# Kernel tuning notes

Measured on AMD Instinct MI355X. Metric: run time of the kernel, lower is better.

The kernel has to match this reference:

```python
import jax, jax.numpy as jnp
import numpy as np

N_NODES = 100000
N_EDGES = 800000
N_REL = 16
D = 64
EPS = 1e-12
NEG_SLOPE = 0.01  # nn.LeakyReLU default


def _l2norm(x):
    # matches torch F.normalize(p=2, dim=-1)
    n = jnp.sqrt(jnp.sum(x * x, axis=-1, keepdims=True))
    return x / jnp.maximum(n, EPS)


def setup_inputs() -> dict:
    key = jax.random.key(0)
    ks = jax.random.split(key, 12)
    inp = {
        "src": jax.random.randint(ks[0], (N_EDGES,), 0, N_NODES, dtype=jnp.int32),
        "dst": jax.random.randint(ks[1], (N_EDGES,), 0, N_NODES, dtype=jnp.int32),
        "etype": jax.random.randint(ks[2], (N_EDGES,), 0, N_REL, dtype=jnp.int32),
        "ent_embed": jax.random.normal(ks[3], (N_NODES, D), jnp.float32) * 0.1,
        "ent_transfer": jax.random.normal(ks[4], (N_NODES, D), jnp.float32) * 0.1,
        "rel_embed": jax.random.normal(ks[5], (N_REL, D), jnp.float32) * 0.1,
        "rel_transfer": jax.random.normal(ks[6], (N_REL, D), jnp.float32) * 0.1,
        "W1_0": jax.random.normal(ks[7], (64, 32), jnp.float32) * (1.0 / np.sqrt(64)),
        "b1_0": jnp.zeros((32,), jnp.float32),
        "W2_0": jax.random.normal(ks[8], (64, 32), jnp.float32) * (1.0 / np.sqrt(64)),
        "b2_0": jnp.zeros((32,), jnp.float32),
        "W1_1": jax.random.normal(ks[9], (32, 16), jnp.float32) * (1.0 / np.sqrt(32)),
        "b1_1": jnp.zeros((16,), jnp.float32),
        "W2_1": jax.random.normal(ks[10], (32, 16), jnp.float32) * (1.0 / np.sqrt(32)),
        "b2_1": jnp.zeros((16,), jnp.float32),
    }
    return inp


def _compute_att(src, dst, etype, ent_embed, ent_transfer, rel_embed, rel_transfer):
    # per-edge gathers: h = dst node, t = src node (KGAT att_score convention)
    h_e = ent_embed[dst]          # [E, D]
    t_e = ent_embed[src]          # [E, D]
    h_p = ent_transfer[dst]
    t_p = ent_transfer[src]
    r_p = rel_transfer[etype]     # [E, D]
    r_e = rel_embed[etype]        # [E, D]
    # TransD projection + L2 normalize
    Mrt = _l2norm(t_e + jnp.sum(t_e * t_p, -1, keepdims=True) * r_p)
    Mrh = _l2norm(h_e + jnp.sum(h_e * h_p, -1, keepdims=True) * r_p)
    att = jnp.sum(Mrt * jnp.tanh(Mrh + r_e), axis=-1)  # [E]
    # edge softmax grouped by destination node
    m = jax.ops.segment_max(att, dst, num_segments=N_NODES)
    m = jnp.where(jnp.isfinite(m), m, 0.0)
    ex = jnp.exp(att - m[dst])
    s = jax.ops.segment_sum(ex, dst, num_segments=N_NODES)
    return ex / jnp.maximum(s[dst], EPS)  # [E]


def _bi_layer(node, N_h, W1, b1, W2, b2):
    out1 = jax.nn.leaky_relu((node + N_h) @ W1 + b1, NEG_SLOPE)
    out2 = jax.nn.leaky_relu((node * N_h) @ W2 + b2, NEG_SLOPE)
    return out1 + out2


def reference(src, dst, etype, ent_embed, ent_transfer, rel_embed, rel_transfer,
              W1_0, b1_0, W2_0, b2_0, W1_1, b1_1, W2_1, b2_1):
    att = _compute_att(src, dst, etype, ent_embed, ent_transfer, rel_embed, rel_transfer)
    node = ent_embed
    all_embed = [node]
    for (W1, b1, W2, b2) in [(W1_0, b1_0, W2_0, b2_0), (W1_1, b1_1, W2_1, b2_1)]:
        # u_mul_e + sum: N_h[v] = sum_{e: dst(e)=v} att_e * node[src(e)]
        msg = att[:, None] * node[src]                      # [E, d]
        N_h = jax.ops.segment_sum(msg, dst, num_segments=N_NODES)
        node = _bi_layer(node, N_h, W1, b1, W2, b2)         # dropout p=0 (eval)
        all_embed.append(_l2norm(node))
    return jnp.concatenate(all_embed, axis=1)  # [N, 64+32+16]
```

## Files before the change

kernel.cpp:

```cpp
#include <hip/hip_runtime.h>
#include <math.h>

#define EPSF 1e-12f
#define LOG2E 1.44269504f

template <int CTRL>
__device__ __forceinline__ float dppadd(float x) {
    union { float f; int i; } u, r;
    u.f = x;
    r.i = __builtin_amdgcn_update_dpp(0, u.i, CTRL, 0xF, 0xF, false);
    return x + r.f;
}
__device__ __forceinline__ float red16(float v) {
    v = dppadd<0xB1>(v); v = dppadd<0x4E>(v);
    v = dppadd<0x141>(v); v = dppadd<0x140>(v);
    return v;
}
__device__ __forceinline__ float red8(float v) {
    v = dppadd<0xB1>(v); v = dppadd<0x4E>(v); v = dppadd<0x141>(v);
    return v;
}
__device__ __forceinline__ float xor8add(float v) {
    return dppadd<0x128>(v);
}

__device__ __forceinline__ float fast_tanh(float x) {
    float E = __builtin_amdgcn_exp2f(x * (2.0f * LOG2E));
    return 1.0f - 2.0f * __builtin_amdgcn_rcpf(E + 1.0f);
}

__device__ __forceinline__ float inv_norm(float x) {
    return __builtin_amdgcn_rsqf(fmaxf(x, 1e-24f));
}

__device__ __forceinline__ float leaky(float x) {
    return x > 0.0f ? x : 0.01f * x;
}

__global__ __launch_bounds__(256) void prep(
    const float* __restrict__ ent, const float* __restrict__ entT,
    float* __restrict__ dot, const int* __restrict__ dst,
    int* __restrict__ deg, int N16, int E,
    const float* __restrict__ W10, const float* __restrict__ W20,
    const float* __restrict__ W11, const float* __restrict__ W21,
    float4* __restrict__ wt) {
    int gid = blockIdx.x * 256 + threadIdx.x;
    if (gid < N16) {
        int v = gid >> 4, lane = gid & 15;
        const float4 a = *(const float4*)(ent  + (size_t)v * 64 + lane * 4);
        const float4 b = *(const float4*)(entT + (size_t)v * 64 + lane * 4);
        float d = red16(a.x*b.x + a.y*b.y + a.z*b.z + a.w*b.w);
        if (lane == 0) dot[v] = d;
    } else if (gid < N16 + E) {
        int e = gid - N16;
        atomicAdd(&deg[dst[e]], 1);
    } else {
        int w = gid - N16 - E;
        if (w < 512) {
            int dd = w >> 5, j = w & 31, d4 = dd * 4;
            wt[w] = make_float4(W10[(d4+0)*32+j], W10[(d4+1)*32+j],
                                W10[(d4+2)*32+j], W10[(d4+3)*32+j]);
        } else if (w < 1024) {
            int u = w - 512, dd = u >> 5, j = u & 31, d4 = dd * 4;
            wt[w] = make_float4(W20[(d4+0)*32+j], W20[(d4+1)*32+j],
                                W20[(d4+2)*32+j], W20[(d4+3)*32+j]);
        } else if (w < 1152) {
            int u = w - 1024, dd = u >> 4, j = u & 15, d4 = dd * 4;
            wt[w] = make_float4(W11[(d4+0)*16+j], W11[(d4+1)*16+j],
                                W11[(d4+2)*16+j], W11[(d4+3)*16+j]);
        } else if (w < 1280) {
            int u = w - 1152, dd = u >> 4, j = u & 15, d4 = dd * 4;
            wt[w] = make_float4(W21[(d4+0)*16+j], W21[(d4+1)*16+j],
                                W21[(d4+2)*16+j], W21[(d4+3)*16+j]);
        }
    }
}


__global__ __launch_bounds__(256) void scan_reduce(
    const int* __restrict__ deg, int* __restrict__ part, int N) {
    __shared__ int sh[256];
    int t = threadIdx.x, i = blockIdx.x * 256 + t;
    sh[t] = (i < N) ? deg[i] : 0;
    __syncthreads();
    for (int off = 128; off > 0; off >>= 1) {
        if (t < off) sh[t] += sh[t + off];
        __syncthreads();
    }
    if (t == 0) part[blockIdx.x] = sh[0];
}

__global__ __launch_bounds__(1024) void scan_part(int* __restrict__ part, int nb) {
    __shared__ int sh[1024];
    int t = threadIdx.x;
    int x = (t < nb) ? part[t] : 0;
    sh[t] = x;
    __syncthreads();
    for (int off = 1; off < 1024; off <<= 1) {
        int y = (t >= off) ? sh[t - off] : 0;
        __syncthreads();
        sh[t] += y;
        __syncthreads();
    }
    if (t < nb) part[t] = sh[t] - x;
}

__global__ __launch_bounds__(256) void scan_write(
    int* __restrict__ rowptr, const int* __restrict__ part, int N) {
    __shared__ int sh[256];
    int t = threadIdx.x, i = blockIdx.x * 256 + t;
    int x = (i < N) ? rowptr[i] : 0;
    sh[t] = x;
    __syncthreads();
    for (int off = 1; off < 256; off <<= 1) {
        int y = (t >= off) ? sh[t - off] : 0;
        __syncthreads();
        sh[t] += y;
        __syncthreads();
    }
    if (i < N) rowptr[i] = part[blockIdx.x] + sh[t] - x;
}

__global__ __launch_bounds__(256) void scatter_edges(
    const int* __restrict__ src, const int* __restrict__ dst,
    const int* __restrict__ ety, const float* __restrict__ dot,
    int* __restrict__ rowptr, int2* __restrict__ spk2, int E) {
    int e = blockIdx.x * 256 + threadIdx.x;
    if (e < E) {
        int sv = src[e];
        int slot = atomicAdd(&rowptr[dst[e]], 1);
        spk2[slot] = make_int2(sv | (ety[e] << 20), __float_as_int(dot[sv]));
    }
}

__global__ __launch_bounds__(256) void fused_l0(
    const int* __restrict__ rowptr, const int2* __restrict__ spk2,
    const float* __restrict__ ent, const float* __restrict__ dot,
    const float* __restrict__ relE, const float* __restrict__ relT,
    const float4* __restrict__ wt,
    const float* __restrict__ b1, const float* __restrict__ b2,
    float* __restrict__ exatt, float* __restrict__ sinv,
    float* __restrict__ node1raw, float* __restrict__ out, int N) {
    __shared__ float  al[8][64];
    __shared__ float  bl[8][64];
    __shared__ float  rT[16][64];
    __shared__ float  rE[16][64];
    __shared__ float4 WtA[512];
    __shared__ float4 WtB[512];
    int t = threadIdx.x;

    {
        int r = t >> 4, c = (t & 15) * 4;
        *(float4*)&rT[r][c] = *(const float4*)(relT + r * 64 + c);
        *(float4*)&rE[r][c] = *(const float4*)(relE + r * 64 + c);
        WtA[t]       = wt[t];
        WtA[t + 256] = wt[t + 256];
        WtB[t]       = wt[512 + t];
        WtB[t + 256] = wt[768 + t];
    }
    __syncthreads();

    int nv = t >> 5, half = (t >> 4) & 1, lane = t & 15;
    int v = blockIdx.x * 8 + nv;
    if (v >= N) return;

    int s = v ? rowptr[v - 1] : 0;
    int epos = rowptr[v];
    int deg = epos - s;
    int mid = s + ((deg + 1) >> 1);
    int hs   = half ? mid  : s;
    int hend = half ? epos : mid;

    const float4 he = *(const float4*)(ent + (size_t)v * 64 + lane * 4);
    float dh = dot[v];

    float4 macc = {0.f, 0.f, 0.f, 0.f};
    float sumex = 0.0f;

    for (int base = hs; base < hend; base += 16) {
        int rem = hend - base;
        int cnt = rem < 16 ? rem : 16;
        int2 ms = spk2[base + (lane < rem ? lane : rem - 1)];
        float myex = 0.0f;

        int pk0 = __shfl(ms.x, 0, 16);
        int pk1 = __shfl(ms.x, cnt > 1 ? 1 : 0, 16);
        float sd0 = __int_as_float(__shfl(ms.y, 0, 16));
        float sd1 = __int_as_float(__shfl(ms.y, cnt > 1 ? 1 : 0, 16));
        float4 te0 = *(const float4*)(ent + (size_t)(pk0 & 0xFFFFF) * 64 + lane * 4);
        float4 te1 = *(const float4*)(ent + (size_t)(pk1 & 0xFFFFF) * 64 + lane * 4);

        for (int k = 0; k < cnt; k += 2) {
            float4 ta = te0, tb = te1;
            float  sa = sd0, sb = sd1;
            int rva = (pk0 >> 20) & 15;
            int rvb = (pk1 >> 20) & 15;
            bool hasb = (k + 1) < cnt;

            if (k + 2 < cnt) {
                int i2 = k + 2, i3 = (k + 3 < cnt) ? (k + 3) : (k + 2);
                pk0 = __shfl(ms.x, i2, 16);
                pk1 = __shfl(ms.x, i3, 16);
                sd0 = __int_as_float(__shfl(ms.y, i2, 16));
                sd1 = __int_as_float(__shfl(ms.y, i3, 16));
                te0 = *(const float4*)(ent + (size_t)(pk0 & 0xFFFFF) * 64 + lane * 4);
                te1 = *(const float4*)(ent + (size_t)(pk1 & 0xFFFFF) * 64 + lane * 4);
            }

            const float4 rpa = *(const float4*)&rT[rva][lane * 4];
            const float4 rea = *(const float4*)&rE[rva][lane * 4];
            const float4 rpb = *(const float4*)&rT[rvb][lane * 4];
            const float4 reb = *(const float4*)&rE[rvb][lane * 4];

            float4 mta, mha, mtb, mhb;
            mta.x = ta.x + sa * rpa.x; mta.y = ta.y + sa * rpa.y;
            mta.z = ta.z + sa * rpa.z; mta.w = ta.w + sa * rpa.w;
            mha.x = he.x + dh * rpa.x; mha.y = he.y + dh * rpa.y;
            mha.z = he.z + dh * rpa.z; mha.w = he.w + dh * rpa.w;
            mtb.x = tb.x + sb * rpb.x; mtb.y = tb.y + sb * rpb.y;
            mtb.z = tb.z + sb * rpb.z; mtb.w = tb.w + sb * rpb.w;
            mhb.x = he.x + dh * rpb.x; mhb.y = he.y + dh * rpb.y;
            mhb.z = he.z + dh * rpb.z; mhb.w = he.w + dh * rpb.w;

            float ssta = red16(mta.x*mta.x + mta.y*mta.y + mta.z*mta.z + mta.w*mta.w);
            float ssha = red16(mha.x*mha.x + mha.y*mha.y + mha.z*mha.z + mha.w*mha.w);
            float sstb = red16(mtb.x*mtb.x + mtb.y*mtb.y + mtb.z*mtb.z + mtb.w*mtb.w);
            float sshb = red16(mhb.x*mhb.x + mhb.y*mhb.y + mhb.z*mhb.z + mhb.w*mhb.w);
            float ita = inv_norm(ssta), iha = inv_norm(ssha);
            float itb = inv_norm(sstb), ihb = inv_norm(sshb);

            float txa = fast_tanh(mha.x * iha + rea.x);
            float tya = fast_tanh(mha.y * iha + rea.y);
            float tza = fast_tanh(mha.z * iha + rea.z);
            float twa = fast_tanh(mha.w * iha + rea.w);
            float txb = fast_tanh(mhb.x * ihb + reb.x);
            float tyb = fast_tanh(mhb.y * ihb + reb.y);
            float tzb = fast_tanh(mhb.z * ihb + reb.z);
            float twb = fast_tanh(mhb.w * ihb + reb.w);

            float atta = ita * red16(mta.x*txa + mta.y*tya + mta.z*tza + mta.w*twa);
            float attb = itb * red16(mtb.x*txb + mtb.y*tyb + mtb.z*tzb + mtb.w*twb);

            float exa  = __builtin_amdgcn_exp2f(atta * LOG2E);
            float exbR = __builtin_amdgcn_exp2f(attb * LOG2E);
            float exb  = hasb ? exbR : 0.0f;

            myex = (lane == k) ? exa : myex;
            myex = (lane == k + 1) ? exbR : myex;

            sumex += exa + exb;
            macc.x += exa * ta.x + exb * tb.x;
            macc.y += exa * ta.y + exb * tb.y;
            macc.z += exa * ta.z + exb * tb.z;
            macc.w += exa * ta.w + exb * tb.w;
        }
        if (lane < cnt) exatt[base + lane] = myex;
    }

    sumex  += __shfl_xor(sumex,  16, 32);
    macc.x += __shfl_xor(macc.x, 16, 32);
    macc.y += __shfl_xor(macc.y, 16, 32);
    macc.z += __shfl_xor(macc.z, 16, 32);
    macc.w += __shfl_xor(macc.w, 16, 32);

    float inv = 1.0f / fmaxf(sumex, EPSF);
    if ((t & 31) == 0) sinv[v] = inv;
    macc.x *= inv; macc.y *= inv; macc.z *= inv; macc.w *= inv;

    if (!half) {
        *(float4*)(out + (size_t)v * 112 + lane * 4) = he;
        float4 av, bv;
        av.x = he.x + macc.x; av.y = he.y + macc.y;
        av.z = he.z + macc.z; av.w = he.w + macc.w;
        bv.x = he.x * macc.x; bv.y = he.y * macc.y;
        bv.z = he.z * macc.z; bv.w = he.w * macc.w;
        *(float4*)&al[nv][lane * 4] = av;
        *(float4*)&bl[nv][lane * 4] = bv;
    }

    int j = t & 31;
    float acc1 = b1[j], acc2 = b2[j];
    #pragma unroll
    for (int dd = 0; dd < 16; ++dd) {
        float4 a4 = *(const float4*)&al[nv][dd * 4];
        float4 b4 = *(const float4*)&bl[nv][dd * 4];
        float4 wa = WtA[dd * 32 + j];
        float4 wb = WtB[dd * 32 + j];
        acc1 += a4.x*wa.x + a4.y*wa.y + a4.z*wa.z + a4.w*wa.w;
        acc2 += b4.x*wb.x + b4.y*wb.y + b4.z*wb.z + b4.w*wb.w;
    }
    node1raw[(size_t)v * 32 + j] = leaky(acc1) + leaky(acc2);
}

__global__ __launch_bounds__(256) void fused_l1(
    const int* __restrict__ rowptr, const int2* __restrict__ spk2,
    const float* __restrict__ exatt, const float* __restrict__ sinv,
    const float* __restrict__ node1raw, const float4* __restrict__ wt,
    const float* __restrict__ b1, const float* __restrict__ b2,
    float* __restrict__ out, int N) {
    __shared__ float  A[16][32];
    __shared__ float  B[16][32];
    __shared__ float4 WtC[128];
    __shared__ float4 WtD[128];
    int t = threadIdx.x;

    {
        if (t < 128) WtC[t] = wt[1024 + t];
        else WtD[t - 128] = wt[1024 + t];
    }
    __syncthreads();

    int nv = t >> 4, half = (t >> 3) & 1, lane = t & 7;
    int v = blockIdx.x * 16 + nv;
    if (v >= N) return;

    int s = v ? rowptr[v - 1] : 0;
    int epos = rowptr[v];
    int deg = epos - s;
    int mid = s + ((deg + 1) >> 1);
    int hs   = half ? mid  : s;
    int hend = half ? epos : mid;

    float4 n = *(const float4*)(node1raw + (size_t)v * 32 + lane * 4);
    float4 acc = {0.f, 0.f, 0.f, 0.f};

    for (int base = hs; base < hend; base += 8) {
        int rem = hend - base;
        int cnt = rem < 8 ? rem : 8;
        int idx = base + (lane < rem ? lane : rem - 1);
        int   mypk = spk2[idx].x;
        float myex = exatt[idx];

        int pk0 = __shfl(mypk, 0, 8);
        int pk1 = __shfl(mypk, cnt > 1 ? 1 : 0, 8);
        float4 x0 = *(const float4*)(node1raw + (size_t)(pk0 & 0xFFFFF) * 32 + lane * 4);
        float4 x1 = *(const float4*)(node1raw + (size_t)(pk1 & 0xFFFFF) * 32 + lane * 4);

        for (int k = 0; k < cnt; k += 2) {
            float4 xa = x0, xb = x1;
            float aa = __shfl(myex, k, 8);
            float ab = __shfl(myex, (k + 1 < cnt) ? (k + 1) : k, 8);
            if (!((k + 1) < cnt)) ab = 0.0f;

            if (k + 2 < cnt) {
                pk0 = __shfl(mypk, k + 2, 8);
                pk1 = __shfl(mypk, (k + 3 < cnt) ? (k + 3) : (k + 2), 8);
                x0 = *(const float4*)(node1raw + (size_t)(pk0 & 0xFFFFF) * 32 + lane * 4);
                x1 = *(const float4*)(node1raw + (size_t)(pk1 & 0xFFFFF) * 32 + lane * 4);
            }
            acc.x += aa * xa.x + ab * xb.x;
            acc.y += aa * xa.y + ab * xb.y;
            acc.z += aa * xa.z + ab * xb.z;
            acc.w += aa * xa.w + ab * xb.w;
        }
    }
    acc.x = xor8add(acc.x);
    acc.y = xor8add(acc.y);
    acc.z = xor8add(acc.z);
    acc.w = xor8add(acc.w);

    float inv = sinv[v];
    acc.x *= inv; acc.y *= inv; acc.z *= inv; acc.w *= inv;

    float ss = red8(n.x*n.x + n.y*n.y + n.z*n.z + n.w*n.w);
    float inv1 = inv_norm(ss);

    if (!half) {
        float4 nn = {n.x*inv1, n.y*inv1, n.z*inv1, n.w*inv1};
        *(float4*)(out + (size_t)v * 112 + 64 + lane * 4) = nn;
        float4 av = {n.x + acc.x, n.y + acc.y, n.z + acc.z, n.w + acc.w};
        float4 bv = {n.x * acc.x, n.y * acc.y, n.z * acc.z, n.w * acc.w};
        *(float4*)&A[nv][lane * 4] = av;
        *(float4*)&B[nv][lane * 4] = bv;
    }

    int j = t & 15;
    float a1 = b1[j], a2 = b2[j];
    #pragma unroll
    for (int dd = 0; dd < 8; ++dd) {
        float4 a4 = *(const float4*)&A[nv][dd * 4];
        float4 b4 = *(const float4*)&B[nv][dd * 4];
        float4 wc = WtC[dd * 16 + j];
        float4 wd = WtD[dd * 16 + j];
        a1 += a4.x*wc.x + a4.y*wc.y + a4.z*wc.z + a4.w*wc.w;
        a2 += b4.x*wd.x + b4.y*wd.y + b4.z*wd.z + b4.w*wd.w;
    }
    float tot = leaky(a1) + leaky(a2);
    float s2 = red16(tot * tot);
    float inv2 = inv_norm(s2);
    out[(size_t)v * 112 + 96 + j] = tot * inv2;
}

extern "C" void kernel_launch(void* const* d_in, const int* in_sizes, int n_in,
                              void* d_out, int out_size, void* d_ws, size_t ws_size,
                              hipStream_t stream) {
    const int*   src  = (const int*)d_in[0];
    const int*   dst  = (const int*)d_in[1];
    const int*   ety  = (const int*)d_in[2];
    const float* ent  = (const float*)d_in[3];
    const float* entT = (const float*)d_in[4];
    const float* relE = (const float*)d_in[5];
    const float* relT = (const float*)d_in[6];
    const float* W1_0 = (const float*)d_in[7];
    const float* b1_0 = (const float*)d_in[8];
    const float* W2_0 = (const float*)d_in[9];
    const float* b2_0 = (const float*)d_in[10];
    const float* W1_1 = (const float*)d_in[11];
    const float* b1_1 = (const float*)d_in[12];
    const float* W2_1 = (const float*)d_in[13];
    const float* b2_1 = (const float*)d_in[14];
    float* out = (float*)d_out;

    const int E = in_sizes[0];
    const int N = in_sizes[3] / 64;
    const int nb = (N + 255) / 256;

    auto al256 = [](size_t x) { return (x + 255) & ~(size_t)255; };
    char* ws = (char*)d_ws;
    size_t offExatt = 0;
    size_t offS     = al256(offExatt + (size_t)E * 4);
    size_t offDot   = al256(offS + (size_t)N * 4);
    size_t offRow   = al256(offDot + (size_t)N * 4);
    size_t offSpk   = al256(offRow + (size_t)N * 4);
    size_t offPart  = al256(offSpk + (size_t)E * 8);
    size_t offN1    = al256(offPart + (size_t)nb * 4);
    size_t offWt    = al256(offN1 + (size_t)N * 32 * 4);
    float*  exatt    = (float*)(ws + offExatt);
    float*  sinv     = (float*)(ws + offS);
    float*  dot      = (float*)(ws + offDot);
    int*    rowptr   = (int*)(ws + offRow);
    int2*   spk2     = (int2*)(ws + offSpk);
    int*    part     = (int*)(ws + offPart);
    float*  node1raw = (float*)(ws + offN1);
    float4* wt       = (float4*)(ws + offWt);

    hipMemsetAsync(rowptr, 0, (size_t)N * 4, stream);
    int N16 = N * 16;
    int prepWork = N16 + E + 1280;
    prep<<<(prepWork + 255) / 256, 256, 0, stream>>>(
        ent, entT, dot, dst, rowptr, N16, E, W1_0, W2_0, W1_1, W2_1, wt);
    scan_reduce<<<nb, 256, 0, stream>>>(rowptr, part, N);
    scan_part<<<1, 1024, 0, stream>>>(part, nb);
    scan_write<<<nb, 256, 0, stream>>>(rowptr, part, N);
    int blkE = (E + 255) / 256;
    scatter_edges<<<blkE, 256, 0, stream>>>(src, dst, ety, dot, rowptr, spk2, E);

    fused_l0<<<(N + 7) / 8, 256, 0, stream>>>(
        rowptr, spk2, ent, dot, relE, relT,
        wt, b1_0, b2_0, exatt, sinv, node1raw, out, N);

    fused_l1<<<(N + 15) / 16, 256, 0, stream>>>(
        rowptr, spk2, exatt, sinv, node1raw, wt,
        b1_1, b2_1, out, N);
}
```

Measured before the change: 207.8 us.

## Precompute TransD projection norms algebraically per edge instead of reducing in-kernel

Expands the squared norm of e + (e·p)·r as |e|² + 2(e·p)(e·r) + (e·p)²|r|², so the per-edge inverse norms come from per-node dot products against the 16 relation vectors plus per-relation norms. Prep now computes |e|² per node and a node×relation table of e·r, and scatter_edges computes both inverse norms per edge and stores them in a widened 16-byte edge record. This removes four 16-lane DPP reductions per edge pair from fused_l0. In exchange the edge records are twice as large, so fused_l0 and fused_l1 read more bytes, scatter_edges does extra random gathers, and the expanded form can lose precision through cancellation.

```diff
diff --git a/kernel.cpp b/kernel.cpp
--- a/kernel.cpp
+++ b/kernel.cpp
@@ -39,8 +39,10 @@
 
 __global__ __launch_bounds__(256) void prep(
     const float* __restrict__ ent, const float* __restrict__ entT,
-    float* __restrict__ dot, const int* __restrict__ dst,
+    float2* __restrict__ dn, const int* __restrict__ dst,
     int* __restrict__ deg, int N16, int E,
+    const float* __restrict__ relT, float* __restrict__ hrp,
+    float* __restrict__ rp2,
     const float* __restrict__ W10, const float* __restrict__ W20,
     const float* __restrict__ W11, const float* __restrict__ W21,
     float4* __restrict__ wt) {
@@ -49,13 +51,36 @@
         int v = gid >> 4, lane = gid & 15;
         const float4 a = *(const float4*)(ent  + (size_t)v * 64 + lane * 4);
         const float4 b = *(const float4*)(entT + (size_t)v * 64 + lane * 4);
-        float d = red16(a.x*b.x + a.y*b.y + a.z*b.z + a.w*b.w);
-        if (lane == 0) dot[v] = d;
+        float d  = red16(a.x*b.x + a.y*b.y + a.z*b.z + a.w*b.w);
+        float n2 = red16(a.x*a.x + a.y*a.y + a.z*a.z + a.w*a.w);
+        if (lane == 0) dn[v] = make_float2(d, n2);
     } else if (gid < N16 + E) {
         int e = gid - N16;
         atomicAdd(&deg[dst[e]], 1);
+    } else if (gid < N16 + E + N16) {
+        int idx = gid - N16 - E;
+        int n = idx >> 4, r = idx & 15;
+        const float4* e4 = (const float4*)(ent + (size_t)n * 64);
+        const float4* w4 = (const float4*)(relT + r * 64);
+        float acc = 0.0f;
+        #pragma unroll
+        for (int k = 0; k < 16; ++k) {
+            float4 a = e4[k], b = w4[k];
+            acc += a.x*b.x + a.y*b.y + a.z*b.z + a.w*b.w;
+        }
+        hrp[n * 16 + r] = acc;
+    } else if (gid < N16 + E + N16 + 16) {
+        int r = gid - N16 - E - N16;
+        const float4* w4 = (const float4*)(relT + r * 64);
+        float acc = 0.0f;
+        #pragma unroll
+        for (int k = 0; k < 16; ++k) {
+            float4 b = w4[k];
+            acc += b.x*b.x + b.y*b.y + b.z*b.z + b.w*b.w;
+        }
+        rp2[r] = acc;
     } else {
-        int w = gid - N16 - E;
+        int w = gid - N16 - E - N16 - 16;
         if (w < 512) {
             int dd = w >> 5, j = w & 31, d4 = dd * 4;
             wt[w] = make_float4(W10[(d4+0)*32+j], W10[(d4+1)*32+j],
@@ -123,19 +148,29 @@
 
 __global__ __launch_bounds__(256) void scatter_edges(
     const int* __restrict__ src, const int* __restrict__ dst,
-    const int* __restrict__ ety, const float* __restrict__ dot,
-    int* __restrict__ rowptr, int2* __restrict__ spk2, int E) {
+    const int* __restrict__ ety, const float2* __restrict__ dn,
+    const float* __restrict__ hrp, const float* __restrict__ rp2,
+    int* __restrict__ rowptr, int4* __restrict__ spk4, int E) {
     int e = blockIdx.x * 256 + threadIdx.x;
     if (e < E) {
-        int sv = src[e];
-        int slot = atomicAdd(&rowptr[dst[e]], 1);
-        spk2[slot] = make_int2(sv | (ety[e] << 20), __float_as_int(dot[sv]));
+        int sv = src[e], dv = dst[e], rv = ety[e];
+        float2 dns = dn[sv], dnd = dn[dv];
+        float hs = hrp[sv * 16 + rv], hd = hrp[dv * 16 + rv];
+        float r2 = rp2[rv];
+        float sdt = dns.x, dh = dnd.x;
+        float sst = dns.y + 2.0f * sdt * hs + sdt * sdt * r2;
+        float ssh = dnd.y + 2.0f * dh  * hd + dh  * dh  * r2;
+        float it = inv_norm(sst);
+        float ih = inv_norm(ssh);
+        int slot = atomicAdd(&rowptr[dv], 1);
+        spk4[slot] = make_int4(sv | (rv << 20), __float_as_int(sdt),
+                               __float_as_int(it), __float_as_int(ih));
     }
 }
 
 __global__ __launch_bounds__(256) void fused_l0(
-    const int* __restrict__ rowptr, const int2* __restrict__ spk2,
-    const float* __restrict__ ent, const float* __restrict__ dot,
+    const int* __restrict__ rowptr, const int4* __restrict__ spk4,
+    const float* __restrict__ ent, const float2* __restrict__ dn,
     const float* __restrict__ relE, const float* __restrict__ relT,
     const float4* __restrict__ wt,
     const float* __restrict__ b1, const float* __restrict__ b2,
@@ -172,7 +207,7 @@
     int hend = half ? epos : mid;
 
     const float4 he = *(const float4*)(ent + (size_t)v * 64 + lane * 4);
-    float dh = dot[v];
+    float dh = dn[v].x;
 
     float4 macc = {0.f, 0.f, 0.f, 0.f};
     float sumex = 0.0f;
@@ -180,19 +215,25 @@
     for (int base = hs; base < hend; base += 16) {
         int rem = hend - base;
         int cnt = rem < 16 ? rem : 16;
-        int2 ms = spk2[base + (lane < rem ? lane : rem - 1)];
+        int4 ms = spk4[base + (lane < rem ? lane : rem - 1)];
         float myex = 0.0f;
 
-        int pk0 = __shfl(ms.x, 0, 16);
-        int pk1 = __shfl(ms.x, cnt > 1 ? 1 : 0, 16);
+        int e1i = cnt > 1 ? 1 : 0;
+        int   pk0 = __shfl(ms.x, 0, 16);
+        int   pk1 = __shfl(ms.x, e1i, 16);
         float sd0 = __int_as_float(__shfl(ms.y, 0, 16));
-        float sd1 = __int_as_float(__shfl(ms.y, cnt > 1 ? 1 : 0, 16));
+        float sd1 = __int_as_float(__shfl(ms.y, e1i, 16));
+        float it0 = __int_as_float(__shfl(ms.z, 0, 16));
+        float it1 = __int_as_float(__shfl(ms.z, e1i, 16));
+        float ih0 = __int_as_float(__shfl(ms.w, 0, 16));
+        float ih1 = __int_as_float(__shfl(ms.w, e1i, 16));
         float4 te0 = *(const float4*)(ent + (size_t)(pk0 & 0xFFFFF) * 64 + lane * 4);
         float4 te1 = *(const float4*)(ent + (size_t)(pk1 & 0xFFFFF) * 64 + lane * 4);
 
         for (int k = 0; k < cnt; k += 2) {
             float4 ta = te0, tb = te1;
             float  sa = sd0, sb = sd1;
+            float ita = it0, itb = it1, iha = ih0, ihb = ih1;
             int rva = (pk0 >> 20) & 15;
             int rvb = (pk1 >> 20) & 15;
             bool hasb = (k + 1) < cnt;
@@ -203,6 +244,10 @@
                 pk1 = __shfl(ms.x, i3, 16);
                 sd0 = __int_as_float(__shfl(ms.y, i2, 16));
                 sd1 = __int_as_float(__shfl(ms.y, i3, 16));
+                it0 = __int_as_float(__shfl(ms.z, i2, 16));
+                it1 = __int_as_float(__shfl(ms.z, i3, 16));
+                ih0 = __int_as_float(__shfl(ms.w, i2, 16));
+                ih1 = __int_as_float(__shfl(ms.w, i3, 16));
                 te0 = *(const float4*)(ent + (size_t)(pk0 & 0xFFFFF) * 64 + lane * 4);
                 te1 = *(const float4*)(ent + (size_t)(pk1 & 0xFFFFF) * 64 + lane * 4);
             }
@@ -221,13 +266,6 @@
             mtb.z = tb.z + sb * rpb.z; mtb.w = tb.w + sb * rpb.w;
             mhb.x = he.x + dh * rpb.x; mhb.y = he.y + dh * rpb.y;
             mhb.z = he.z + dh * rpb.z; mhb.w = he.w + dh * rpb.w;
-
-            float ssta = red16(mta.x*mta.x + mta.y*mta.y + mta.z*mta.z + mta.w*mta.w);
-            float ssha = red16(mha.x*mha.x + mha.y*mha.y + mha.z*mha.z + mha.w*mha.w);
-            float sstb = red16(mtb.x*mtb.x + mtb.y*mtb.y + mtb.z*mtb.z + mtb.w*mtb.w);
-            float sshb = red16(mhb.x*mhb.x + mhb.y*mhb.y + mhb.z*mhb.z + mhb.w*mhb.w);
-            float ita = inv_norm(ssta), iha = inv_norm(ssha);
-            float itb = inv_norm(sstb), ihb = inv_norm(sshb);
 
             float txa = fast_tanh(mha.x * iha + rea.x);
             float tya = fast_tanh(mha.y * iha + rea.y);
@@ -293,7 +331,7 @@
 }
 
 __global__ __launch_bounds__(256) void fused_l1(
-    const int* __restrict__ rowptr, const int2* __restrict__ spk2,
+    const int* __restrict__ rowptr, const int4* __restrict__ spk4,
     const float* __restrict__ exatt, const float* __restrict__ sinv,
     const float* __restrict__ node1raw, const float4* __restrict__ wt,
     const float* __restrict__ b1, const float* __restrict__ b2,
@@ -328,7 +366,7 @@
         int rem = hend - base;
         int cnt = rem < 8 ? rem : 8;
         int idx = base + (lane < rem ? lane : rem - 1);
-        int   mypk = spk2[idx].x;
+        int   mypk = spk4[idx].x;
         float myex = exatt[idx];
 
         int pk0 = __shfl(mypk, 0, 8);
@@ -418,38 +456,44 @@
     auto al256 = [](size_t x) { return (x + 255) & ~(size_t)255; };
     char* ws = (char*)d_ws;
     size_t offExatt = 0;
-    size_t offS     = al256(offExatt + (size_t)E * 4);
-    size_t offDot   = al256(offS + (size_t)N * 4);
-    size_t offRow   = al256(offDot + (size_t)N * 4);
+    size_t offDn    = al256(offExatt + (size_t)E * 4);
+    size_t offS     = al256(offDn + (size_t)N * 8);
+    size_t offRow   = al256(offS + (size_t)N * 4);
     size_t offSpk   = al256(offRow + (size_t)N * 4);
-    size_t offPart  = al256(offSpk + (size_t)E * 8);
+    size_t offHrp   = al256(offSpk + (size_t)E * 16);
+    size_t offRp2   = al256(offHrp + (size_t)N * 16 * 4);
+    size_t offPart  = al256(offRp2 + 16 * 4);
     size_t offN1    = al256(offPart + (size_t)nb * 4);
     size_t offWt    = al256(offN1 + (size_t)N * 32 * 4);
     float*  exatt    = (float*)(ws + offExatt);
+    float2* dn       = (float2*)(ws + offDn);
     float*  sinv     = (float*)(ws + offS);
-    float*  dot      = (float*)(ws + offDot);
     int*    rowptr   = (int*)(ws + offRow);
-    int2*   spk2     = (int2*)(ws + offSpk);
+    int4*   spk4     = (int4*)(ws + offSpk);
+    float*  hrp      = (float*)(ws + offHrp);
+    float*  rp2      = (float*)(ws + offRp2);
     int*    part     = (int*)(ws + offPart);
     float*  node1raw = (float*)(ws + offN1);
     float4* wt       = (float4*)(ws + offWt);
 
     hipMemsetAsync(rowptr, 0, (size_t)N * 4, stream);
     int N16 = N * 16;
-    int prepWork = N16 + E + 1280;
+    int prepWork = N16 + E + N16 + 16 + 1280;
     prep<<<(prepWork + 255) / 256, 256, 0, stream>>>(
-        ent, entT, dot, dst, rowptr, N16, E, W1_0, W2_0, W1_1, W2_1, wt);
+        ent, entT, dn, dst, rowptr, N16, E, relT, hrp, rp2,
+        W1_0, W2_0, W1_1, W2_1, wt);
     scan_reduce<<<nb, 256, 0, stream>>>(rowptr, part, N);
     scan_part<<<1, 1024, 0, stream>>>(part, nb);
     scan_write<<<nb, 256, 0, stream>>>(rowptr, part, N);
     int blkE = (E + 255) / 256;
-    scatter_edges<<<blkE, 256, 0, stream>>>(src, dst, ety, dot, rowptr, spk2, E);
+    scatter_edges<<<blkE, 256, 0, stream>>>(src, dst, ety, dn, hrp, rp2,
+                                            rowptr, spk4, E);
 
     fused_l0<<<(N + 7) / 8, 256, 0, stream>>>(
-        rowptr, spk2, ent, dot, relE, relT,
+        rowptr, spk4, ent, dn, relE, relT,
         wt, b1_0, b2_0, exatt, sinv, node1raw, out, N);
 
     fused_l1<<<(N + 15) / 16, 256, 0, stream>>>(
-        rowptr, spk2, exatt, sinv, node1raw, wt,
+        rowptr, spk4, exatt, sinv, node1raw, wt,
         b1_1, b2_1, out, N);
 }
```

Result: slower. 254.7 us (+22.5%).
